# Kernel tuning notes

Hardware: AMD Instinct MI355X
Metric: run time of the kernel (lower is better)

## Reference

```python
import jax, jax.numpy as jnp
import numpy as np

SUPPORT_RADIUS = 0.1
NUM_BASIS = 7
GRID_MIN, GRID_MAX = -1.5, 1.5
KNN_K = 8
EPS_COV = 1e-14

GRID = jnp.linspace(GRID_MIN, GRID_MAX, NUM_BASIS)          # [7]
H = (GRID_MAX - GRID_MIN) / (NUM_BASIS - 1)                  # 0.5


def _hat(v):
    # v: [..., 1] broadcast against grid -> [..., 7]
    return jax.nn.relu(1.0 - jnp.abs(v - GRID) / H)


def _kan(kan_in, W1a, W1b, W2):
    # kan_in: [P, 2]
    b0 = _hat(kan_in[:, 0:1])                 # [P, 7]
    b1 = _hat(kan_in[:, 1:2])                 # [P, 7]
    hidden = b0 @ W1a.T + b1 @ W1b.T          # [P, 16]
    bh = _hat(hidden[:, :, None])             # [P, 16, 7]
    return bh.reshape(kan_in.shape[0], -1) @ W2.T   # [P, 1]


def _cubic_window(dist, radius):
    q = dist / radius
    inner = 2.0 / 3.0 - 4.0 * q ** 2 + 4.0 * q ** 3
    outer = 4.0 / 3.0 - 4.0 * q + 4.0 * q ** 2 - (4.0 / 3.0) * q ** 3
    return jnp.where(q <= 0.5, inner, jnp.where(q <= 1.0, outer, 0.0))


def _forward(x, nodes, W1a, W1b, W2, w):
    B = x.shape[0]
    N = nodes.shape[0]
    diff = x[:, None, :] - nodes[None, :, :]              # [B, N, 2]
    dist = jnp.linalg.norm(diff, axis=2)                  # [B, N]
    kan_in = (diff / SUPPORT_RADIUS).reshape(-1, 2)       # [B*N, 2]
    phi_raw = jax.nn.softplus(_kan(kan_in, W1a, W1b, W2).reshape(B, N))
    phi_windowed = phi_raw * _cubic_window(dist, SUPPORT_RADIUS)
    phi_sum = jnp.sum(phi_windowed, axis=1, keepdims=True)          # [B, 1]
    orphan = jnp.abs(phi_sum[:, 0]) < EPS_COV                       # [B]
    phi_normal = phi_windowed / (phi_sum + 1e-12)
    # kNN fallback (computed for all rows, selected by orphan mask)
    k = min(KNN_K, N)
    neg_d, idx = jax.lax.top_k(-dist, k)                            # smallest-k
    d_knn = -neg_d                                                  # [B, k]
    alpha = 20.0 / max(SUPPORT_RADIUS, 1e-12)
    wts = jnp.exp(-alpha * d_knn)
    wts = wts / (jnp.sum(wts, axis=1, keepdims=True) + 1e-18)
    rows = jnp.arange(B)[:, None]
    phi_knn = jnp.zeros((B, N), dtype=x.dtype).at[rows, idx].set(wts)
    phi = jnp.where(orphan[:, None], phi_knn, phi_normal)
    return phi @ w                                                   # [B, 1]


def setup_inputs() -> dict:
    key = jax.random.key(0)
    ks = jax.random.split(key, 6)
    return {
        "x": jax.random.uniform(ks[0], (1024, 2), dtype=jnp.float32),
        "nodes": jax.random.uniform(ks[1], (2048, 2), dtype=jnp.float32),
        "W1a": jax.random.normal(ks[2], (16, 7), dtype=jnp.float32) * 0.3,
        "W1b": jax.random.normal(ks[3], (16, 7), dtype=jnp.float32) * 0.3,
        "W2": jax.random.normal(ks[4], (1, 112), dtype=jnp.float32) * 0.1,
        "w": jax.random.normal(ks[5], (2048, 1), dtype=jnp.float32),
    }


def reference(x, nodes, W1a, W1b, W2, w):
    return _forward(x, nodes, W1a, W1b, W2, w)
```

## Files before the change

### kernel.cpp

```cpp
#include <hip/hip_runtime.h>
#include <math.h>


constexpr int NB    = 7;
constexpr int NH    = 16;
constexpr int BLOCK = 256;
constexpr int NMAX  = 2048;

__global__ __launch_bounds__(BLOCK) void meshfree_kan_fwd(
    const float* __restrict__ x,
    const float* __restrict__ nodes,
    const float* __restrict__ W1a,
    const float* __restrict__ W1b,
    const float* __restrict__ W2,
    const float* __restrict__ w,
    float* __restrict__ out,
    int N)
{
    __shared__ float sW1a[NH * NB];
    __shared__ float sW1b[NH * NB];
    __shared__ float sW2 [NH * NB];
    __shared__ float sd2 [NMAX];
    __shared__ int   shidx[NMAX];
    __shared__ int   hcount;
    __shared__ float sred[2][BLOCK / 64];

    const int tid = threadIdx.x;
    const int b   = blockIdx.x;

    for (int i = tid; i < NH * NB; i += BLOCK) {
        sW1a[i] = W1a[i];
        sW1b[i] = W1b[i];
        sW2[i]  = W2[i];
    }
    if (tid == 0) hcount = 0;
    const float xb0 = x[2 * b + 0];
    const float xb1 = x[2 * b + 1];
    __syncthreads();

    for (int base = 0; base < N; base += BLOCK) {
        const int n = base + tid;
        if (n < N) {
            const float2 nd = ((const float2*)nodes)[n];
            const float dx = xb0 - nd.x;
            const float dy = xb1 - nd.y;
            const float d2 = dx * dx + dy * dy;
            sd2[n] = d2;
            if (d2 <= 0.0100000019f) {
                const int p = atomicAdd(&hcount, 1);
                shidx[p] = n;
            }
        }
    }
    __syncthreads();
    const int H = hcount;

    float sum_phi  = 0.0f;
    float sum_phiw = 0.0f;

    for (int k = tid; k < H; k += BLOCK) {
        const int n = shidx[k];
        const float2 nd = ((const float2*)nodes)[n];
        const float dx = xb0 - nd.x;
        const float dy = xb1 - nd.y;
        const float dist = sqrtf(dx * dx + dy * dy);
        const float q  = dist * 10.0f;
        const float kx = dx * 10.0f;
        const float ky = dy * 10.0f;

        const float u0 = (kx + 1.5f) * 2.0f;
        const float f0 = floorf(u0);
        const int   j0 = (int)f0;
        const float t0 = u0 - f0;
        const float u1 = (ky + 1.5f) * 2.0f;
        const float f1 = floorf(u1);
        const int   j1 = (int)f1;
        const float t1 = u1 - f1;

        float acc = 0.0f;
        #pragma unroll
        for (int h = 0; h < NH; ++h) {
            const float hid =
                sW1a[h * NB + j0]     * (1.0f - t0) +
                sW1a[h * NB + j0 + 1] * t0 +
                sW1b[h * NB + j1]     * (1.0f - t1) +
                sW1b[h * NB + j1 + 1] * t1;
            const float uh = (hid + 1.5f) * 2.0f;
            const float fh = floorf(uh);
            const int   jh = (int)fh;
            const float th = uh - fh;
            const float c0 = ((unsigned)jh       <= 6u) ? sW2[h * NB + jh]     : 0.0f;
            const float c1 = ((unsigned)(jh + 1) <= 6u) ? sW2[h * NB + jh + 1] : 0.0f;
            acc += c0 * (1.0f - th) + c1 * th;
        }

        const float phi_raw = fmaxf(acc, 0.0f) + log1pf(expf(-fabsf(acc)));
        float wnd;
        if (q <= 0.5f) {
            wnd = 2.0f / 3.0f - 4.0f * q * q + 4.0f * q * q * q;
        } else if (q <= 1.0f) {
            wnd = 4.0f / 3.0f - 4.0f * q + 4.0f * q * q - (4.0f / 3.0f) * q * q * q;
        } else {
            wnd = 0.0f;
        }
        const float phi = phi_raw * wnd;
        sum_phi  += phi;
        sum_phiw += phi * w[n];
    }

    float v0 = sum_phi, v1 = sum_phiw;
    #pragma unroll
    for (int off = 32; off > 0; off >>= 1) {
        v0 += __shfl_down(v0, off, 64);
        v1 += __shfl_down(v1, off, 64);
    }
    const int wave = tid >> 6;
    if ((tid & 63) == 0) {
        sred[0][wave] = v0;
        sred[1][wave] = v1;
    }
    __syncthreads();

    if (tid == 0) {
        float ps = 0.0f, pw = 0.0f;
        #pragma unroll
        for (int i = 0; i < BLOCK / 64; ++i) {
            ps += sred[0][i];
            pw += sred[1][i];
        }
        float result;
        if (fabsf(ps) >= 1e-14f) {
            result = pw / (ps + 1e-12f);
        } else {
            float dsel[8];
            int   isel[8];
            for (int k = 0; k < 8; ++k) {
                float md = INFINITY;
                int   mi = 0;
                for (int n = 0; n < N; ++n) {
                    const float d = sd2[n];
                    if (d < md) { md = d; mi = n; }
                }
                dsel[k] = sqrtf(md);
                isel[k] = mi;
                sd2[mi] = INFINITY;
            }
            float wts[8];
            float s = 0.0f;
            for (int k = 0; k < 8; ++k) {
                wts[k] = expf(-200.0f * dsel[k]);
                s += wts[k];
            }
            float r = 0.0f;
            for (int k = 0; k < 8; ++k)
                r += (wts[k] / (s + 1e-18f)) * w[isel[k]];
            result = r;
        }
        out[b] = result;
    }
}

extern "C" void kernel_launch(void* const* d_in, const int* in_sizes, int n_in,
                              void* d_out, int out_size, void* d_ws, size_t ws_size,
                              hipStream_t stream) {
    const float* x     = (const float*)d_in[0];
    const float* nodes = (const float*)d_in[1];
    const float* W1a   = (const float*)d_in[2];
    const float* W1b   = (const float*)d_in[3];
    const float* W2    = (const float*)d_in[4];
    const float* w     = (const float*)d_in[5];
    float* out = (float*)d_out;

    const int B = in_sizes[0] / 2;
    const int N = in_sizes[1] / 2;

    meshfree_kan_fwd<<<B, BLOCK, 0, stream>>>(x, nodes, W1a, W1b, W2, w, out, N);
}
```

Baseline: 67.67 us.

## Process four query points per block with a packed shared hit list

```diff
diff --git a/kernel.cpp b/kernel.cpp
--- a/kernel.cpp
+++ b/kernel.cpp
@@ -5,7 +5,8 @@
 constexpr int NB    = 7;
 constexpr int NH    = 16;
 constexpr int BLOCK = 256;
-constexpr int NMAX  = 2048;
+constexpr int QPB   = 4;
+constexpr int CAP   = 4096;
 
 __global__ __launch_bounds__(BLOCK) void meshfree_kan_fwd(
     const float* __restrict__ x,
@@ -15,18 +16,18 @@
     const float* __restrict__ W2,
     const float* __restrict__ w,
     float* __restrict__ out,
-    int N)
+    int B, int N)
 {
     __shared__ float sW1a[NH * NB];
     __shared__ float sW1b[NH * NB];
     __shared__ float sW2 [NH * NB];
-    __shared__ float sd2 [NMAX];
-    __shared__ int   shidx[NMAX];
+    __shared__ int   slist[CAP];
     __shared__ int   hcount;
-    __shared__ float sred[2][BLOCK / 64];
+    __shared__ float sacc[QPB][2];
+    __shared__ float sx[QPB][2];
 
-    const int tid = threadIdx.x;
-    const int b   = blockIdx.x;
+    const int tid   = threadIdx.x;
+    const int qbase = blockIdx.x * QPB;
 
     for (int i = tid; i < NH * NB; i += BLOCK) {
         sW1a[i] = W1a[i];
@@ -34,37 +35,49 @@
         sW2[i]  = W2[i];
     }
     if (tid == 0) hcount = 0;
-    const float xb0 = x[2 * b + 0];
-    const float xb1 = x[2 * b + 1];
+    if (tid < QPB) {
+        sacc[tid][0] = 0.0f;
+        sacc[tid][1] = 0.0f;
+        const int b = qbase + tid;
+        if (b < B) {
+            sx[tid][0] = x[2 * b + 0];
+            sx[tid][1] = x[2 * b + 1];
+        }
+    }
     __syncthreads();
+
+    const int nq = min(QPB, B - qbase);
 
     for (int base = 0; base < N; base += BLOCK) {
         const int n = base + tid;
         if (n < N) {
             const float2 nd = ((const float2*)nodes)[n];
-            const float dx = xb0 - nd.x;
-            const float dy = xb1 - nd.y;
-            const float d2 = dx * dx + dy * dy;
-            sd2[n] = d2;
-            if (d2 <= 0.0100000019f) {
-                const int p = atomicAdd(&hcount, 1);
-                shidx[p] = n;
+            #pragma unroll
+            for (int q = 0; q < QPB; ++q) {
+                if (q < nq) {
+                    const float dx = sx[q][0] - nd.x;
+                    const float dy = sx[q][1] - nd.y;
+                    const float d2 = dx * dx + dy * dy;
+                    if (d2 <= 0.0100000019f) {
+                        const int p = atomicAdd(&hcount, 1);
+                        if (p < CAP) slist[p] = (q << 16) | n;
+                    }
+                }
             }
         }
     }
     __syncthreads();
-    const int H = hcount;
-
-    float sum_phi  = 0.0f;
-    float sum_phiw = 0.0f;
+    const int H = min(hcount, CAP);
 
     for (int k = tid; k < H; k += BLOCK) {
-        const int n = shidx[k];
+        const int e = slist[k];
+        const int q = e >> 16;
+        const int n = e & 0xffff;
         const float2 nd = ((const float2*)nodes)[n];
-        const float dx = xb0 - nd.x;
-        const float dy = xb1 - nd.y;
+        const float dx = sx[q][0] - nd.x;
+        const float dy = sx[q][1] - nd.y;
         const float dist = sqrtf(dx * dx + dy * dy);
-        const float q  = dist * 10.0f;
+        const float qq = dist * 10.0f;
         const float kx = dx * 10.0f;
         const float ky = dy * 10.0f;
 
@@ -96,62 +109,58 @@
 
         const float phi_raw = fmaxf(acc, 0.0f) + log1pf(expf(-fabsf(acc)));
         float wnd;
-        if (q <= 0.5f) {
-            wnd = 2.0f / 3.0f - 4.0f * q * q + 4.0f * q * q * q;
-        } else if (q <= 1.0f) {
-            wnd = 4.0f / 3.0f - 4.0f * q + 4.0f * q * q - (4.0f / 3.0f) * q * q * q;
+        if (qq <= 0.5f) {
+            wnd = 2.0f / 3.0f - 4.0f * qq * qq + 4.0f * qq * qq * qq;
+        } else if (qq <= 1.0f) {
+            wnd = 4.0f / 3.0f - 4.0f * qq + 4.0f * qq * qq
+                  - (4.0f / 3.0f) * qq * qq * qq;
         } else {
             wnd = 0.0f;
         }
         const float phi = phi_raw * wnd;
-        sum_phi  += phi;
-        sum_phiw += phi * w[n];
-    }
-
-    float v0 = sum_phi, v1 = sum_phiw;
-    #pragma unroll
-    for (int off = 32; off > 0; off >>= 1) {
-        v0 += __shfl_down(v0, off, 64);
-        v1 += __shfl_down(v1, off, 64);
-    }
-    const int wave = tid >> 6;
-    if ((tid & 63) == 0) {
-        sred[0][wave] = v0;
-        sred[1][wave] = v1;
+        atomicAdd(&sacc[q][0], phi);
+        atomicAdd(&sacc[q][1], phi * w[n]);
     }
     __syncthreads();
 
-    if (tid == 0) {
-        float ps = 0.0f, pw = 0.0f;
-        #pragma unroll
-        for (int i = 0; i < BLOCK / 64; ++i) {
-            ps += sred[0][i];
-            pw += sred[1][i];
-        }
+    if (tid < nq) {
+        const int b = qbase + tid;
+        const float ps = sacc[tid][0];
         float result;
         if (fabsf(ps) >= 1e-14f) {
-            result = pw / (ps + 1e-12f);
+            result = sacc[tid][1] / (ps + 1e-12f);
         } else {
+            const float qx = sx[tid][0];
+            const float qy = sx[tid][1];
             float dsel[8];
             int   isel[8];
+            #pragma unroll 1
             for (int k = 0; k < 8; ++k) {
                 float md = INFINITY;
                 int   mi = 0;
                 for (int n = 0; n < N; ++n) {
-                    const float d = sd2[n];
-                    if (d < md) { md = d; mi = n; }
+                    const float2 nd = ((const float2*)nodes)[n];
+                    const float dx = qx - nd.x;
+                    const float dy = qy - nd.y;
+                    float d2 = dx * dx + dy * dy;
+                    bool seen = false;
+                    #pragma unroll
+                    for (int j = 0; j < 8; ++j)
+                        if (j < k && isel[j] == n) seen = true;
+                    if (!seen && d2 < md) { md = d2; mi = n; }
                 }
                 dsel[k] = sqrtf(md);
                 isel[k] = mi;
-                sd2[mi] = INFINITY;
             }
             float wts[8];
             float s = 0.0f;
+            #pragma unroll
             for (int k = 0; k < 8; ++k) {
                 wts[k] = expf(-200.0f * dsel[k]);
                 s += wts[k];
             }
             float r = 0.0f;
+            #pragma unroll
             for (int k = 0; k < 8; ++k)
                 r += (wts[k] / (s + 1e-18f)) * w[isel[k]];
             result = r;
@@ -174,5 +183,7 @@
     const int B = in_sizes[0] / 2;
     const int N = in_sizes[1] / 2;
 
-    meshfree_kan_fwd<<<B, BLOCK, 0, stream>>>(x, nodes, W1a, W1b, W2, w, out, N);
+    const int grid = (B + QPB - 1) / QPB;
+    meshfree_kan_fwd<<<grid, BLOCK, 0, stream>>>(x, nodes, W1a, W1b, W2, w,
+                                                 out, B, N);
 }
```

New measurement: 73.90 us. 9.2% more time.
